# Kernel tuning notes

Hardware: AMD Instinct MI355X
Metric: run time of the kernel (lower is better)

The kernel has to match this reference:

```python
import jax, jax.numpy as jnp
import numpy as np

N, T, D, H = 128, 128, 1024, 1024


def setup_inputs() -> dict:
    key = jax.random.key(0)
    ks = jax.random.split(key, 5)
    x = jax.random.normal(ks[0], (N, T, D), dtype=jnp.float32)
    A = jax.random.normal(ks[1], (N, H, 4, 4), dtype=jnp.float32)
    Wx = jax.random.normal(ks[2], (D, 4 * H), dtype=jnp.float32) / np.sqrt(D)
    Wh = jax.random.normal(ks[3], (H, 4 * H), dtype=jnp.float32) / np.sqrt(H)
    Wattn = jax.random.normal(ks[4], (H, 4 * H), dtype=jnp.float32) / np.sqrt(H)
    b = jnp.zeros((4 * H,), dtype=jnp.float32)
    return {"x": x, "A": A, "Wx": Wx, "Wh": Wh, "Wattn": Wattn, "b": b}


def reference(x, A, Wx, Wh, Wattn, b):
    n, t, d = x.shape
    h_dim = A.shape[1]
    scale = 1.0 / (h_dim ** 0.5)
    A_flat = A.reshape(n, h_dim, 16)            # (N, H, 16) flattened 4x4 grid
    h0 = A_flat.mean(axis=2)                    # mean-pooled feature init
    c0 = h0

    def step(carry, xt):
        h, c = carry
        # scaled dot-product attention over the 16 spatial positions
        scores = jnp.einsum('nh,nhp->np', h, A_flat) * scale   # (N, 16)
        w = jax.nn.softmax(scores, axis=-1)
        attn = jnp.einsum('nhp,np->nh', A_flat, w)             # (N, H)
        # fused gate pre-activations
        a = h @ Wh + xt @ Wx + attn @ Wattn + b                # (N, 4H)
        ai, af, ao, ag = jnp.split(a, 4, axis=1)
        i = jax.nn.sigmoid(ai)
        f = jax.nn.sigmoid(af)
        o = jax.nn.sigmoid(ao)
        g = jnp.tanh(ag)
        nc = f * c + i * g
        nh = o * jnp.tanh(nc)
        return (nh, nc), nh

    _, hs = jax.lax.scan(step, (h0, c0), jnp.transpose(x, (1, 0, 2)))
    return jnp.transpose(hs, (1, 0, 2))         # (N, T, H)
```

## Files before the change

kernel.cpp:

```cpp
#include <hip/hip_runtime.h>
#include <hip/hip_bf16.h>


typedef __bf16 bf16x8 __attribute__((ext_vector_type(8)));
typedef float f32x4 __attribute__((ext_vector_type(4)));

__device__ __forceinline__ unsigned short f2bf(float f) {
    unsigned int u = __float_as_uint(f);
    u += 0x7FFFu + ((u >> 16) & 1u);
    return (unsigned short)(u >> 16);
}
__device__ __forceinline__ float bf2f(unsigned short u) {
    return __uint_as_float(((unsigned int)u) << 16);
}
__device__ __forceinline__ float sigf(float x) { return 1.0f / (1.0f + __expf(-x)); }
__device__ __forceinline__ float tanhf_fast(float x) {
    const float t = __expf(-2.0f * fabsf(x));
    const float r = (1.0f - t) / (1.0f + t);
    return copysignf(r, x);
}

__global__ __launch_bounds__(256) void k_build_wtf2(
    const float* __restrict__ Wh, const float* __restrict__ Wx,
    unsigned short* __restrict__ WTf) {
    __shared__ float tile[64][65];
    const int cs2 = blockIdx.x;
    const int kq  = blockIdx.y;
    const int tid = threadIdx.x;
#pragma unroll
    for (int it = 0; it < 16; ++it) {
        int idx = it * 256 + tid;
        int kl = idx >> 6, cl = idx & 63;
        int col = cs2 * 64 + cl;
        int j = (col & 3) * 1024 + (col >> 2);
        int k = kq * 64 + kl;
        tile[kl][cl] = (k < 1024) ? Wh[(size_t)k * 4096 + j]
                                  : Wx[(size_t)(k - 1024) * 4096 + j];
    }
    __syncthreads();
#pragma unroll
    for (int it = 0; it < 2; ++it) {
        int slotid = it * 256 + tid;
        int l   = slotid & 63;
        int cf  = (slotid >> 6) & 1;
        int ksl = (slotid >> 7) & 1;
        int sl  = slotid >> 8;
        int s = cs2 * 2 + sl, ks = kq * 2 + ksl;
        int clocal = sl * 32 + cf * 16 + (l & 15);
        int klocal = ksl * 32 + ((l >> 4) << 3);
        unsigned short v[8];
#pragma unroll
        for (int i = 0; i < 8; ++i) v[i] = f2bf(tile[klocal + i][clocal]);
        *(int4*)&WTf[(size_t)(((s * 64 + ks) * 2 + cf) * 64 + l) * 8] = *(const int4*)v;
    }
}

__global__ __launch_bounds__(256) void k_build_waf(
    const float* __restrict__ Wattn, unsigned short* __restrict__ WAf) {
    __shared__ float tile[64][65];
    const int cs2 = blockIdx.x;
    const int kq  = blockIdx.y;
    const int tid = threadIdx.x;
#pragma unroll
    for (int it = 0; it < 16; ++it) {
        int idx = it * 256 + tid;
        int kl = idx >> 6, cl = idx & 63;
        int col = cs2 * 64 + cl;
        int j = (col & 3) * 1024 + (col >> 2);
        int k = kq * 64 + kl;
        tile[kl][cl] = Wattn[(size_t)k * 4096 + j];
    }
    __syncthreads();
#pragma unroll
    for (int it = 0; it < 2; ++it) {
        int slotid = it * 256 + tid;
        int l   = slotid & 63;
        int cf  = (slotid >> 6) & 1;
        int ksl = (slotid >> 7) & 1;
        int sl  = slotid >> 8;
        int s = cs2 * 2 + sl, ks = kq * 2 + ksl;
        int clocal = sl * 32 + cf * 16 + (l & 15);
        int klocal = ksl * 32 + ((l >> 4) << 3);
        unsigned short v[8];
#pragma unroll
        for (int i = 0; i < 8; ++i) v[i] = f2bf(tile[klocal + i][clocal]);
        *(int4*)&WAf[(size_t)(((s * 32 + ks) * 2 + cf) * 64 + l) * 8] = *(const int4*)v;
    }
}

__global__ __launch_bounds__(256) void k_pack_at(
    const float* __restrict__ Ag, unsigned short* __restrict__ ATf) {
    __shared__ unsigned short lds[1024][17];
    const int n = blockIdx.x;
    const int tid = threadIdx.x;
#pragma unroll
    for (int it = 0; it < 16; ++it) {
        int idx = it * 256 + tid;
        const float4 v = ((const float4*)(Ag + (size_t)n * 16384))[idx];
        int flat = idx * 4;
        int u = flat >> 4, p = flat & 15;
        lds[u][p + 0] = f2bf(v.x); lds[u][p + 1] = f2bf(v.y);
        lds[u][p + 2] = f2bf(v.z); lds[u][p + 3] = f2bf(v.w);
    }
    __syncthreads();
#pragma unroll
    for (int it = 0; it < 8; ++it) {
        int slot = it * 256 + tid;
        int kc = slot >> 6, l = slot & 63;
        int ubase = kc * 32 + ((l >> 4) << 3);
        int p = l & 15;
        unsigned short v[8];
#pragma unroll
        for (int i = 0; i < 8; ++i) v[i] = lds[ubase + i][p];
        *(int4*)&ATf[((size_t)n * 2048 + slot) * 8] = *(const int4*)v;
    }
}

__global__ __launch_bounds__(512) void k_aw_gemm(
    const unsigned short* __restrict__ ATf, const unsigned short* __restrict__ WAf,
    unsigned short* __restrict__ AW) {
    const int ng = blockIdx.x;
    const int ct = blockIdx.y;
    const int tid = threadIdx.x;
    const int lane = tid & 63, wave = tid >> 6;
    const int s = ct * 4 + (wave >> 1), cf = wave & 1;
    const int n0 = ng * 8;
    f32x4 acc[8] = {};
    const unsigned short* bp = WAf + ((size_t)((s * 32) * 2 + cf) * 64 + lane) * 8;
    const unsigned short* ap = ATf + ((size_t)n0 * 2048 + lane) * 8;
#pragma unroll 4
    for (int kc = 0; kc < 32; ++kc) {
        bf16x8 bf = *(const bf16x8*)(bp + (size_t)kc * 1024);
#pragma unroll
        for (int nn = 0; nn < 8; ++nn) {
            bf16x8 af = *(const bf16x8*)(ap + (size_t)nn * 16384 + (size_t)kc * 512);
            acc[nn] = __builtin_amdgcn_mfma_f32_16x16x32_bf16(af, bf, acc[nn], 0, 0, 0);
        }
    }
    const int col = ct * 128 + wave * 16 + (lane & 15);
    const int prow = (lane >> 4) << 2;
#pragma unroll
    for (int nn = 0; nn < 8; ++nn) {
        ushort4 st = make_ushort4(f2bf(acc[nn][0]), f2bf(acc[nn][1]),
                                  f2bf(acc[nn][2]), f2bf(acc[nn][3]));
        *(ushort4*)&AW[((size_t)(n0 + nn) * 4096 + col) * 16 + prow] = st;
    }
}

__global__ __launch_bounds__(512) void k_build_aw(
    const float* __restrict__ Wattn, const float* __restrict__ Ag,
    unsigned short* __restrict__ AW) {
    extern __shared__ float Alds[];
    const int jt = blockIdx.x;
    const int ng = blockIdx.y;
    const int tid = threadIdx.x;
    const int jl = tid & 127, pg = tid >> 7;
    const int jj = jt * 128 + jl;
    for (int nn = 0; nn < 16; ++nn) {
        const int n = ng * 16 + nn;
        __syncthreads();
#pragma unroll
        for (int q = 0; q < 8; ++q) {
            int idx = q * 512 + tid;
            ((float4*)Alds)[idx] = ((const float4*)(Ag + (size_t)n * 16384))[idx];
        }
        __syncthreads();
        f32x4 acc = {0.f, 0.f, 0.f, 0.f};
#pragma unroll 8
        for (int u = 0; u < 1024; ++u) {
            float wv = Wattn[(size_t)u * 4096 + jj];
            const float4 av = *(const float4*)&Alds[u * 16 + pg * 4];
            acc[0] += wv * av.x; acc[1] += wv * av.y;
            acc[2] += wv * av.z; acc[3] += wv * av.w;
        }
        const int g = jj >> 10, unit = jj & 1023;
        const int cre = unit * 4 + g;
        ushort4 st = make_ushort4(f2bf(acc[0]), f2bf(acc[1]), f2bf(acc[2]), f2bf(acc[3]));
        *(ushort4*)&AW[((size_t)n * 4096 + cre) * 16 + pg * 4] = st;
    }
}

__global__ __launch_bounds__(512) void k_init(
    const float* __restrict__ Ag, float* __restrict__ cst,
    unsigned short* __restrict__ hF0, float* __restrict__ sp) {
    const int n = blockIdx.x;
    const int t = threadIdx.x;
    float contrib[16];
#pragma unroll
    for (int p = 0; p < 16; ++p) contrib[p] = 0.f;
#pragma unroll
    for (int e = 0; e < 2; ++e) {
        const int u = t * 2 + e;
        const float4* ap = (const float4*)&Ag[((size_t)n * 1024 + u) * 16];
        float4 a0 = ap[0], a1 = ap[1], a2 = ap[2], a3 = ap[3];
        float s = a0.x + a0.y + a0.z + a0.w + a1.x + a1.y + a1.z + a1.w +
                  a2.x + a2.y + a2.z + a2.w + a3.x + a3.y + a3.z + a3.w;
        float h0 = s * (1.0f / 16.0f);
        cst[n * 1024 + u] = h0;
        const int rfg = n >> 4, kc = u >> 5, l = (n & 15) | (((u >> 3) & 3) << 4);
        hF0[(size_t)((rfg * 32 + kc) * 64 + l) * 8 + (u & 7)] = f2bf(h0);
        contrib[0]  += h0 * a0.x;  contrib[1]  += h0 * a0.y;
        contrib[2]  += h0 * a0.z;  contrib[3]  += h0 * a0.w;
        contrib[4]  += h0 * a1.x;  contrib[5]  += h0 * a1.y;
        contrib[6]  += h0 * a1.z;  contrib[7]  += h0 * a1.w;
        contrib[8]  += h0 * a2.x;  contrib[9]  += h0 * a2.y;
        contrib[10] += h0 * a2.z;  contrib[11] += h0 * a2.w;
        contrib[12] += h0 * a3.x;  contrib[13] += h0 * a3.y;
        contrib[14] += h0 * a3.z;  contrib[15] += h0 * a3.w;
    }
#pragma unroll
    for (int p = 0; p < 16; ++p) {
        contrib[p] += __shfl_xor(contrib[p], 1);
        contrib[p] += __shfl_xor(contrib[p], 2);
    }
    if ((t & 3) == 0) {
        const int slice = t >> 2;
        float4* dst = (float4*)&sp[(size_t)n * 4096 + slice * 16];
        dst[0] = make_float4(contrib[0], contrib[1], contrib[2], contrib[3]);
        dst[1] = make_float4(contrib[4], contrib[5], contrib[6], contrib[7]);
        dst[2] = make_float4(contrib[8], contrib[9], contrib[10], contrib[11]);
        dst[3] = make_float4(contrib[12], contrib[13], contrib[14], contrib[15]);
    }
    *(float4*)&sp[(size_t)n * 4096 + 2048 + t * 4] = make_float4(0.f, 0.f, 0.f, 0.f);
}

__global__ __launch_bounds__(64) void k_soft(
    const float* __restrict__ spin, float* __restrict__ w_ws,
    const float* __restrict__ x, unsigned short* __restrict__ xf, int ts) {
    __shared__ float sq[16];
    const int n = blockIdx.x;
    const int lane = threadIdx.x;
    f32x4 acc = {0.f, 0.f, 0.f, 0.f};
    const float4* base = (const float4*)(spin + (size_t)n * 4096);
#pragma unroll
    for (int it = 0; it < 16; ++it) {
        const float4 v = base[it * 64 + lane];
        acc[0] += v.x; acc[1] += v.y; acc[2] += v.z; acc[3] += v.w;
    }
#pragma unroll
    for (int m = 4; m <= 32; m <<= 1) {
        acc[0] += __shfl_xor(acc[0], m);
        acc[1] += __shfl_xor(acc[1], m);
        acc[2] += __shfl_xor(acc[2], m);
        acc[3] += __shfl_xor(acc[3], m);
    }
    if (lane < 4) *(float4*)&sq[lane * 4] = make_float4(acc[0], acc[1], acc[2], acc[3]);
    __syncthreads();
    if (lane < 16) {
        const float s = sq[lane] * 0.03125f;
        float mx = s;
#pragma unroll
        for (int m = 1; m < 16; m <<= 1) mx = fmaxf(mx, __shfl_xor(mx, m));
        const float e = __expf(s - mx);
        float se = e;
#pragma unroll
        for (int m = 1; m < 16; m <<= 1) se += __shfl_xor(se, m);
        w_ws[n * 16 + lane] = e / se;
    }
    const float4* xp = (const float4*)&x[((size_t)n * 128 + ts) * 1024];
#pragma unroll
    for (int i = 0; i < 2; ++i) {
        const int js = lane * 2 + i;
        const float4 x0 = xp[js * 2], x1 = xp[js * 2 + 1];
        unsigned short v[8] = {f2bf(x0.x), f2bf(x0.y), f2bf(x0.z), f2bf(x0.w),
                               f2bf(x1.x), f2bf(x1.y), f2bf(x1.z), f2bf(x1.w)};
        const int j0 = js * 8;
        const int l = (n & 15) | (((j0 >> 3) & 3) << 4);
        *(int4*)&xf[(size_t)(((n >> 4) * 32 + (j0 >> 5)) * 64 + l) * 8] = *(const int4*)v;
    }
}

__global__ __launch_bounds__(512) void k_step(
    const unsigned short* __restrict__ WTf, const unsigned short* __restrict__ AW,
    const unsigned short* __restrict__ hFin, unsigned short* __restrict__ hFout,
    const unsigned short* __restrict__ xf,
    const float* __restrict__ w_ws, float* __restrict__ spout,
    float* __restrict__ cst, const float* __restrict__ Ag,
    const float* __restrict__ bias4, float* __restrict__ out, int ts) {
    __shared__ float wlds[64][17];
    __shared__ float accred[2048];
    const int bid = blockIdx.x;
    const int cs = bid >> 1, rh = bid & 1;
    const int tid = threadIdx.x;
    const int lane = tid & 63, wave = tid >> 6;
    const int rf = wave & 3, kh = wave >> 2;

    f32x4 acc0 = {0.f, 0.f, 0.f, 0.f}, acc1 = {0.f, 0.f, 0.f, 0.f};
    {
        const unsigned short* ap = (kh == 0 ? hFin : xf)
            + ((size_t)((rh * 4 + rf) * 32) * 64 + lane) * 8;
        const unsigned short* bp = WTf
            + ((size_t)((cs * 64 + kh * 32) * 2) * 64 + lane) * 8;
        bf16x8 ax[4], bx0[4], bx1[4], ay[4], by0[4], by1[4];
#pragma unroll
        for (int i = 0; i < 4; ++i) {
            ax[i]  = *(const bf16x8*)(ap + (size_t)i * 512);
            bx0[i] = *(const bf16x8*)(bp + (size_t)i * 1024);
            bx1[i] = *(const bf16x8*)(bp + (size_t)i * 1024 + 512);
        }
#pragma unroll
        for (int kb = 0; kb < 32; kb += 8) {
#pragma unroll
            for (int i = 0; i < 4; ++i) {
                const int kc = kb + 4 + i;
                ay[i]  = *(const bf16x8*)(ap + (size_t)kc * 512);
                by0[i] = *(const bf16x8*)(bp + (size_t)kc * 1024);
                by1[i] = *(const bf16x8*)(bp + (size_t)kc * 1024 + 512);
            }
#pragma unroll
            for (int i = 0; i < 4; ++i) {
                acc0 = __builtin_amdgcn_mfma_f32_16x16x32_bf16(ax[i], bx0[i], acc0, 0, 0, 0);
                acc1 = __builtin_amdgcn_mfma_f32_16x16x32_bf16(ax[i], bx1[i], acc1, 0, 0, 0);
            }
            if (kb + 8 < 32) {
#pragma unroll
                for (int i = 0; i < 4; ++i) {
                    const int kc = kb + 8 + i;
                    ax[i]  = *(const bf16x8*)(ap + (size_t)kc * 512);
                    bx0[i] = *(const bf16x8*)(bp + (size_t)kc * 1024);
                    bx1[i] = *(const bf16x8*)(bp + (size_t)kc * 1024 + 512);
                }
            }
#pragma unroll
            for (int i = 0; i < 4; ++i) {
                acc0 = __builtin_amdgcn_mfma_f32_16x16x32_bf16(ay[i], by0[i], acc0, 0, 0, 0);
                acc1 = __builtin_amdgcn_mfma_f32_16x16x32_bf16(ay[i], by1[i], acc1, 0, 0, 0);
            }
        }
    }

    const int lq = lane & 15;
    const int hi = lane >> 4;
    const int mycol = cs * 32 + kh * 16 + lq;
    const int u = mycol >> 2, g = mycol & 3;
    int4 aw0[4], aw1[4];
    float cold[4];
#pragma unroll
    for (int reg = 0; reg < 4; ++reg) {
        const int r = rh * 64 + rf * 16 + hi * 4 + reg;
        const int4* awv = (const int4*)&AW[((size_t)r * 4096 + mycol) * 16];
        aw0[reg] = awv[0];
        aw1[reg] = awv[1];
        cold[reg] = cst[r * 1024 + u];
    }
#pragma unroll
    for (int it = 0; it < 2; ++it) {
        const int idx = it * 512 + tid;
        wlds[idx >> 4][idx & 15] = w_ws[(rh * 64 + (idx >> 4)) * 16 + (idx & 15)];
    }
    const f32x4 accoth = (kh == 0) ? acc1 : acc0;
    *(f32x4*)&accred[((rf * 2 + kh) * 64 + lane) * 4] = accoth;
    __syncthreads();
    f32x4 acc = (kh == 0) ? acc0 : acc1;
    acc += *(const f32x4*)&accred[((rf * 2 + (kh ^ 1)) * 64 + lane) * 4];

    const float bias = bias4[g * 1024 + u];
    float nhv[4];
#pragma unroll
    for (int reg = 0; reg < 4; ++reg) {
        const int r = rh * 64 + rf * 16 + hi * 4 + reg;
        const int rl = rf * 16 + hi * 4 + reg;
        union { int4 v; unsigned short us[8]; } a0u, a1u;
        a0u.v = aw0[reg]; a1u.v = aw1[reg];
        float aextra = 0.f;
#pragma unroll
        for (int p = 0; p < 8; ++p) aextra += wlds[rl][p] * bf2f(a0u.us[p]);
#pragma unroll
        for (int p = 0; p < 8; ++p) aextra += wlds[rl][8 + p] * bf2f(a1u.us[p]);
        float a = acc[reg] + bias + aextra;
        float v1 = __shfl_xor(a, 1);
        float v2 = __shfl_xor(a, 2);
        float v3 = __shfl_xor(a, 3);
        auto pick = [&](int m) { return m == 0 ? a : m == 1 ? v1 : m == 2 ? v2 : v3; };
        float ii = sigf(pick(g));
        float ff = sigf(pick(g ^ 1));
        float oo = sigf(pick(g ^ 2));
        float gg = tanhf_fast(pick(g ^ 3));
        const float nc = ff * cold[reg] + ii * gg;
        const float nh = oo * tanhf_fast(nc);
        nhv[reg] = nh;
        if (g == 0) {
            cst[r * 1024 + u] = nc;
        } else if (g == 1) {
            hFout[(size_t)(((r >> 4) * 32 + (u >> 5)) * 64 +
                           ((r & 15) | (((u >> 3) & 3) << 4))) * 8 + (u & 7)] = f2bf(nh);
        } else if (g == 3) {
            out[((size_t)r * 128 + ts) * 1024 + u] = nh;
        }
    }
    if ((lq & 3) == 2) {
#pragma unroll
        for (int reg = 0; reg < 4; ++reg) {
            const int r = rh * 64 + rf * 16 + hi * 4 + reg;
            const float nh = nhv[reg];
            const float4* Ap = (const float4*)&Ag[((size_t)r * 1024 + u) * 16];
            float contrib[16];
#pragma unroll
            for (int q = 0; q < 4; ++q) {
                const float4 cv = Ap[q];
                contrib[q * 4 + 0] = nh * cv.x;
                contrib[q * 4 + 1] = nh * cv.y;
                contrib[q * 4 + 2] = nh * cv.z;
                contrib[q * 4 + 3] = nh * cv.w;
            }
#pragma unroll
            for (int p = 0; p < 16; ++p) {
                contrib[p] += __shfl_xor(contrib[p], 4);
                contrib[p] += __shfl_xor(contrib[p], 8);
            }
            if (lq == 2) {
                float4* dst = (float4*)&spout[((size_t)r * 256 + (cs * 2 + kh)) * 16];
                dst[0] = make_float4(contrib[0], contrib[1], contrib[2], contrib[3]);
                dst[1] = make_float4(contrib[4], contrib[5], contrib[6], contrib[7]);
                dst[2] = make_float4(contrib[8], contrib[9], contrib[10], contrib[11]);
                dst[3] = make_float4(contrib[12], contrib[13], contrib[14], contrib[15]);
            }
        }
    }
}

extern "C" void kernel_launch(void* const* d_in, const int* in_sizes, int n_in,
                              void* d_out, int out_size, void* d_ws, size_t ws_size,
                              hipStream_t stream) {
    const float* x     = (const float*)d_in[0];
    const float* A     = (const float*)d_in[1];
    const float* Wx    = (const float*)d_in[2];
    const float* Wh    = (const float*)d_in[3];
    const float* Wattn = (const float*)d_in[4];
    const float* b     = (const float*)d_in[5];
    float* out = (float*)d_out;

    char* ws = (char*)d_ws;
    unsigned short* WTf = (unsigned short*)(ws);
    unsigned short* AW  = (unsigned short*)(ws + 16777216);
    unsigned short* hF0 = (unsigned short*)(ws + 33554432);
    unsigned short* hF1 = (unsigned short*)(ws + 33816576);
    unsigned short* xf  = (unsigned short*)(ws + 34078720);
    float* cst  = (float*)(ws + 34340864);
    float* w_ws = (float*)(ws + 34865152);
    float* sp0  = (float*)(ws + 34873344);
    float* sp1  = (float*)(ws + 36970496);
    unsigned short* ATf = (unsigned short*)(ws + 33554432);
    unsigned short* WAf = (unsigned short*)(ws + 37748736);

    k_build_wtf2<<<dim3(64, 32), 256, 0, stream>>>(Wh, Wx, WTf);
    if (ws_size >= 46137344u) {
        k_build_waf<<<dim3(64, 16), 256, 0, stream>>>(Wattn, WAf);
        k_pack_at<<<128, 256, 0, stream>>>(A, ATf);
        k_aw_gemm<<<dim3(16, 32), 512, 0, stream>>>(ATf, WAf, AW);
    } else {
        k_build_aw<<<dim3(32, 8), 512, 65536, stream>>>(Wattn, A, AW);
    }
    k_init<<<128, 512, 0, stream>>>(A, cst, hF0, sp0);

    for (int ts = 0; ts < 128; ++ts) {
        unsigned short* hin  = (ts & 1) ? hF1 : hF0;
        unsigned short* hout = (ts & 1) ? hF0 : hF1;
        float* spin  = (ts & 1) ? sp1 : sp0;
        float* spout = (ts & 1) ? sp0 : sp1;
        k_soft<<<128, 64, 0, stream>>>(spin, w_ws, x, xf, ts);
        k_step<<<256, 512, 0, stream>>>(WTf, AW, hin, hout, xf,
                                        w_ws, spout, cst, A, b, out, ts);
    }
}
```

Measured before the change: 2.561 ms.

## Split step kernel across twice as many blocks with single-tile waves and XCD-aware remap

Each k_step block now computes a 16-column tile instead of 32 columns, so the grid doubles to 512 blocks and each wave issues a single accumulator chain with an 8-deep register prefetch ring. Waves are regrouped so the two K-halves sit in adjacent waves, and each wave finishes only 2 of the 4 output rows after the LDS reduction. Block IDs are remapped with a stride of 8 so neighbouring column tiles share an XCD's L2, and launch bounds request higher occupancy. The aim is more CUs busy on the latency-bound per-timestep GEMM, at the cost of A-operand loads duplicated across more blocks and a longer serial MFMA chain per wave.

```diff
diff --git a/kernel.cpp b/kernel.cpp
--- a/kernel.cpp
+++ b/kernel.cpp
@@ -270,7 +270,7 @@
     }
 }
 
-__global__ __launch_bounds__(512) void k_step(
+__global__ __launch_bounds__(512, 4) void k_step(
     const unsigned short* __restrict__ WTf, const unsigned short* __restrict__ AW,
     const unsigned short* __restrict__ hFin, unsigned short* __restrict__ hFout,
     const unsigned short* __restrict__ xf,
@@ -279,89 +279,69 @@
     const float* __restrict__ bias4, float* __restrict__ out, int ts) {
     __shared__ float wlds[64][17];
     __shared__ float accred[2048];
-    const int bid = blockIdx.x;
-    const int cs = bid >> 1, rh = bid & 1;
+    const int bid0 = blockIdx.x;
+    const int lid = (bid0 & 7) * 64 + (bid0 >> 3);
+    const int cs16 = lid >> 1, rh = lid & 1;
     const int tid = threadIdx.x;
     const int lane = tid & 63, wave = tid >> 6;
-    const int rf = wave & 3, kh = wave >> 2;
-
-    f32x4 acc0 = {0.f, 0.f, 0.f, 0.f}, acc1 = {0.f, 0.f, 0.f, 0.f};
+    const int rf = wave >> 1, kh = wave & 1;
+
+    f32x4 acc = {0.f, 0.f, 0.f, 0.f};
     {
         const unsigned short* ap = (kh == 0 ? hFin : xf)
             + ((size_t)((rh * 4 + rf) * 32) * 64 + lane) * 8;
         const unsigned short* bp = WTf
-            + ((size_t)((cs * 64 + kh * 32) * 2) * 64 + lane) * 8;
-        bf16x8 ax[4], bx0[4], bx1[4], ay[4], by0[4], by1[4];
-#pragma unroll
-        for (int i = 0; i < 4; ++i) {
-            ax[i]  = *(const bf16x8*)(ap + (size_t)i * 512);
-            bx0[i] = *(const bf16x8*)(bp + (size_t)i * 1024);
-            bx1[i] = *(const bf16x8*)(bp + (size_t)i * 1024 + 512);
-        }
-#pragma unroll
-        for (int kb = 0; kb < 32; kb += 8) {
-#pragma unroll
-            for (int i = 0; i < 4; ++i) {
-                const int kc = kb + 4 + i;
-                ay[i]  = *(const bf16x8*)(ap + (size_t)kc * 512);
-                by0[i] = *(const bf16x8*)(bp + (size_t)kc * 1024);
-                by1[i] = *(const bf16x8*)(bp + (size_t)kc * 1024 + 512);
+            + ((size_t)((((cs16 >> 1) * 64 + kh * 32) * 2) + (cs16 & 1)) * 64 + lane) * 8;
+        bf16x8 ar[8], br[8];
+#pragma unroll
+        for (int i = 0; i < 8; ++i) {
+            ar[i] = *(const bf16x8*)(ap + (size_t)i * 512);
+            br[i] = *(const bf16x8*)(bp + (size_t)i * 1024);
+        }
+#pragma unroll
+        for (int kb = 0; kb < 32; ++kb) {
+            bf16x8 a = ar[kb & 7], b = br[kb & 7];
+            if (kb < 24) {
+                ar[kb & 7] = *(const bf16x8*)(ap + (size_t)(kb + 8) * 512);
+                br[kb & 7] = *(const bf16x8*)(bp + (size_t)(kb + 8) * 1024);
             }
-#pragma unroll
-            for (int i = 0; i < 4; ++i) {
-                acc0 = __builtin_amdgcn_mfma_f32_16x16x32_bf16(ax[i], bx0[i], acc0, 0, 0, 0);
-                acc1 = __builtin_amdgcn_mfma_f32_16x16x32_bf16(ax[i], bx1[i], acc1, 0, 0, 0);
-            }
-            if (kb + 8 < 32) {
-#pragma unroll
-                for (int i = 0; i < 4; ++i) {
-                    const int kc = kb + 8 + i;
-                    ax[i]  = *(const bf16x8*)(ap + (size_t)kc * 512);
-                    bx0[i] = *(const bf16x8*)(bp + (size_t)kc * 1024);
-                    bx1[i] = *(const bf16x8*)(bp + (size_t)kc * 1024 + 512);
-                }
-            }
-#pragma unroll
-            for (int i = 0; i < 4; ++i) {
-                acc0 = __builtin_amdgcn_mfma_f32_16x16x32_bf16(ay[i], by0[i], acc0, 0, 0, 0);
-                acc1 = __builtin_amdgcn_mfma_f32_16x16x32_bf16(ay[i], by1[i], acc1, 0, 0, 0);
-            }
+            acc = __builtin_amdgcn_mfma_f32_16x16x32_bf16(a, b, acc, 0, 0, 0);
         }
     }
 
     const int lq = lane & 15;
     const int hi = lane >> 4;
-    const int mycol = cs * 32 + kh * 16 + lq;
+    const int mycol = cs16 * 16 + lq;
     const int u = mycol >> 2, g = mycol & 3;
-    int4 aw0[4], aw1[4];
-    float cold[4];
-#pragma unroll
-    for (int reg = 0; reg < 4; ++reg) {
+    int4 aw0[2], aw1[2];
+    float cold[2];
+#pragma unroll
+    for (int e = 0; e < 2; ++e) {
+        const int reg = kh * 2 + e;
         const int r = rh * 64 + rf * 16 + hi * 4 + reg;
         const int4* awv = (const int4*)&AW[((size_t)r * 4096 + mycol) * 16];
-        aw0[reg] = awv[0];
-        aw1[reg] = awv[1];
-        cold[reg] = cst[r * 1024 + u];
+        aw0[e] = awv[0];
+        aw1[e] = awv[1];
+        cold[e] = cst[r * 1024 + u];
     }
 #pragma unroll
     for (int it = 0; it < 2; ++it) {
         const int idx = it * 512 + tid;
         wlds[idx >> 4][idx & 15] = w_ws[(rh * 64 + (idx >> 4)) * 16 + (idx & 15)];
     }
-    const f32x4 accoth = (kh == 0) ? acc1 : acc0;
-    *(f32x4*)&accred[((rf * 2 + kh) * 64 + lane) * 4] = accoth;
+    *(f32x4*)&accred[(wave * 64 + lane) * 4] = acc;
     __syncthreads();
-    f32x4 acc = (kh == 0) ? acc0 : acc1;
-    acc += *(const f32x4*)&accred[((rf * 2 + (kh ^ 1)) * 64 + lane) * 4];
+    acc += *(const f32x4*)&accred[(((rf << 1) | (kh ^ 1)) * 64 + lane) * 4];
 
     const float bias = bias4[g * 1024 + u];
-    float nhv[4];
-#pragma unroll
-    for (int reg = 0; reg < 4; ++reg) {
+    float nhv[2];
+#pragma unroll
+    for (int e = 0; e < 2; ++e) {
+        const int reg = kh * 2 + e;
         const int r = rh * 64 + rf * 16 + hi * 4 + reg;
         const int rl = rf * 16 + hi * 4 + reg;
         union { int4 v; unsigned short us[8]; } a0u, a1u;
-        a0u.v = aw0[reg]; a1u.v = aw1[reg];
+        a0u.v = aw0[e]; a1u.v = aw1[e];
         float aextra = 0.f;
 #pragma unroll
         for (int p = 0; p < 8; ++p) aextra += wlds[rl][p] * bf2f(a0u.us[p]);
@@ -376,9 +356,9 @@
         float ff = sigf(pick(g ^ 1));
         float oo = sigf(pick(g ^ 2));
         float gg = tanhf_fast(pick(g ^ 3));
-        const float nc = ff * cold[reg] + ii * gg;
+        const float nc = ff * cold[e] + ii * gg;
         const float nh = oo * tanhf_fast(nc);
-        nhv[reg] = nh;
+        nhv[e] = nh;
         if (g == 0) {
             cst[r * 1024 + u] = nc;
         } else if (g == 1) {
@@ -390,9 +370,10 @@
     }
     if ((lq & 3) == 2) {
 #pragma unroll
-        for (int reg = 0; reg < 4; ++reg) {
+        for (int e = 0; e < 2; ++e) {
+            const int reg = kh * 2 + e;
             const int r = rh * 64 + rf * 16 + hi * 4 + reg;
-            const float nh = nhv[reg];
+            const float nh = nhv[e];
             const float4* Ap = (const float4*)&Ag[((size_t)r * 1024 + u) * 16];
             float contrib[16];
 #pragma unroll
@@ -409,7 +390,7 @@
                 contrib[p] += __shfl_xor(contrib[p], 8);
             }
             if (lq == 2) {
-                float4* dst = (float4*)&spout[((size_t)r * 256 + (cs * 2 + kh)) * 16];
+                float4* dst = (float4*)&spout[((size_t)r * 256 + cs16) * 16];
                 dst[0] = make_float4(contrib[0], contrib[1], contrib[2], contrib[3]);
                 dst[1] = make_float4(contrib[4], contrib[5], contrib[6], contrib[7]);
                 dst[2] = make_float4(contrib[8], contrib[9], contrib[10], contrib[11]);
@@ -459,7 +440,7 @@
         float* spin  = (ts & 1) ? sp1 : sp0;
         float* spout = (ts & 1) ? sp0 : sp1;
         k_soft<<<128, 64, 0, stream>>>(spin, w_ws, x, xf, ts);
-        k_step<<<256, 512, 0, stream>>>(WTf, AW, hin, hout, xf,
+        k_step<<<512, 512, 0, stream>>>(WTf, AW, hin, hout, xf,
                                         w_ws, spout, cst, A, b, out, ts);
     }
 }
```

Measured after the change: 2.661 ms. +3.9%, slower.
